# Kernel tuning notes

Hardware: AMD Instinct MI355X
Metric: run time of the kernel (lower is better)

The kernel has to match this reference:

```python
import jax, jax.numpy as jnp
import numpy as np

N_NODES = 1024
N_EDGES = 32768
FEAT = 384
HID = 64
OUT = 64


def setup_inputs() -> dict:
    key = jax.random.key(0)
    ks = jax.random.split(key, 10)
    features = jax.random.normal(ks[0], (N_NODES, FEAT), dtype=jnp.float32)
    edge_index = jax.random.randint(ks[1], (2, N_EDGES), 0, N_NODES, dtype=jnp.int64 if jax.config.jax_enable_x64 else jnp.int32)
    edge_attr = jax.random.uniform(ks[2], (N_EDGES, 1), dtype=jnp.float32)
    # Linear weights (stored as [in, out]; torch Linear does x @ W.T)
    sc = 1.0 / np.sqrt(FEAT)
    Wk = jax.random.uniform(ks[3], (FEAT, HID), dtype=jnp.float32, minval=-sc, maxval=sc)
    Wq = jax.random.uniform(ks[4], (FEAT, HID), dtype=jnp.float32, minval=-sc, maxval=sc)
    Wv = jax.random.uniform(ks[5], (FEAT, OUT), dtype=jnp.float32, minval=-sc, maxval=sc)
    # Embedding tables, init N(0, 1)
    Ek = jax.random.normal(ks[6], (2, HID), dtype=jnp.float32)
    Eq = jax.random.normal(ks[7], (2, HID), dtype=jnp.float32)
    Ev = jax.random.normal(ks[8], (2, OUT), dtype=jnp.float32)
    bias = jnp.full((1,), 0.5, dtype=jnp.float32)
    mult = jnp.full((1,), 10.0, dtype=jnp.float32)
    return {"features": features, "edge_index": edge_index, "edge_attr": edge_attr,
            "Wk": Wk, "Wq": Wq, "Wv": Wv, "Ek": Ek, "Eq": Eq, "Ev": Ev,
            "bias": bias, "mult": mult}


def _dense_adj(src, dst, vals, n, d):
    # torch_geometric.utils.to_dense_adj: scatter-add edge attrs into [N, N, d]
    return jnp.zeros((n, n, d), vals.dtype).at[src, dst].add(vals)


def reference(features, edge_index, edge_attr, Wk, Wq, Wv, Ek, Eq, Ev, bias, mult):
    N, L = features.shape
    k = features @ Wk                      # [N, H]
    q = features @ Wq                      # [N, H]
    v = features @ Wv                      # [N, O]

    # ContinuousEmbeddingIndex: sigmoid interp, weights [E, 2]
    w = jax.nn.sigmoid((edge_attr - bias) * mult)
    w = jnp.concatenate([w, 1.0 - w], axis=-1)

    src, dst = edge_index[0], edge_index[1]
    A = q @ k.T                            # [N, N]

    # key relative embeddings (original casts to int64 -> truncate toward 0)
    rk = jnp.trunc(w @ Ek)                 # [E, H]
    Rk = _dense_adj(src, dst, rk, N, Ek.shape[1])
    A = A + jnp.einsum('ih,ijh->ij', q, Rk)

    # query relative embeddings (also truncated)
    rq = jnp.trunc(w @ Eq)
    Rq = _dense_adj(src, dst, rq, N, Eq.shape[1])
    A = A + jnp.einsum('jh,ijh->ij', k, Rq)

    # term3: (q_repeat * k_repeat).sum(-1) == q @ k.T again
    A = A + q @ k.T

    A = jax.nn.softmax(A / jnp.sqrt(jnp.asarray(L, A.dtype)), axis=-1)
    # dropout is identity at inference
    M = A @ v

    # value relative embeddings (float, no truncation)
    rv = w @ Ev                            # [E, O]
    Rv = _dense_adj(src, dst, rv, N, Ev.shape[1])
    M = M + jnp.einsum('ij,ijd->id', A, Rv)
    return M
```

## Files before the change

kernel.cpp:

```cpp
#include <hip/hip_runtime.h>
#include <math.h>

#define N_NODES 1024
#define N_EDGES 32768
#define FEAT    384
#define INV_S   0.05103103630798287f
#define MAXH    1024

__global__ __launch_bounds__(384) void k_kqv(
        const float* __restrict__ feat,
        const float* __restrict__ Wk, const float* __restrict__ Wq,
        const float* __restrict__ Wv,
        float* __restrict__ q, float* __restrict__ k, float* __restrict__ v) {
    __shared__ float fs[4 * FEAT];
    const int tid = threadIdx.x;
    const int row0 = blockIdx.x * 4;
    ((float4*)fs)[tid] = ((const float4*)(feat + (size_t)row0 * FEAT))[tid];
    __syncthreads();
    const int mat = tid >> 7;
    const int sub = tid & 127;
    const int col = sub & 63;
    const int rh  = sub >> 6;
    const float* W  = (mat == 0) ? Wq : (mat == 1 ? Wk : Wv);
    const float* f0 = fs + (rh * 2) * FEAT;
    const float* f1 = fs + (rh * 2 + 1) * FEAT;
    float a0 = 0.f, a1 = 0.f;
    #pragma unroll 8
    for (int f = 0; f < FEAT; ++f) {
        float wv = W[f * 64 + col];
        a0 = fmaf(f0[f], wv, a0);
        a1 = fmaf(f1[f], wv, a1);
    }
    float* out = (mat == 0) ? q : (mat == 1 ? k : v);
    out[(row0 + rh * 2 + 0) * 64 + col] = a0;
    out[(row0 + rh * 2 + 1) * 64 + col] = a1;
}

__global__ __launch_bounds__(512) void k_mega(
        const float* __restrict__ q, const float* __restrict__ k,
        const float* __restrict__ v,
        const int* __restrict__ ei, const float* __restrict__ eattr,
        const float* __restrict__ Ek, const float* __restrict__ Eq,
        const float* __restrict__ Ev,
        const float* __restrict__ bias, const float* __restrict__ mult,
        float* __restrict__ M) {
    __shared__ __align__(16) float As[4][N_NODES];
    __shared__ float qr[4][64];
    __shared__ __align__(16) float scratch[2048];
    __shared__ float redm[8], reds[8];
    __shared__ float sS[4][2];
    __shared__ int nhit;
    int*   list  = (int*)scratch;
    float* wlist = scratch + 1024;
    float* red   = scratch;

    const int tid  = threadIdx.x;
    const int lane = tid & 63;
    const int wave = tid >> 6;
    const int row0 = blockIdx.x * 4;

    if (tid < 8) ((float*)sS)[tid] = 0.f;
    if (tid == 8) nhit = 0;
    if (tid < 256) qr[tid >> 6][tid & 63] = q[row0 * 64 + tid];
    __syncthreads();

    {
        const int4* s4 = (const int4*)ei;
        #pragma unroll 4
        for (int it = 0; it < 16; ++it) {
            const int i4 = tid + it * 512;
            const int4 sv = s4[i4];
            const int eb = i4 * 4;
            if ((unsigned)(sv.x - row0) < 4u) { int p = atomicAdd(&nhit, 1); if (p < MAXH) list[p] = eb + 0; }
            if ((unsigned)(sv.y - row0) < 4u) { int p = atomicAdd(&nhit, 1); if (p < MAXH) list[p] = eb + 1; }
            if ((unsigned)(sv.z - row0) < 4u) { int p = atomicAdd(&nhit, 1); if (p < MAXH) list[p] = eb + 2; }
            if ((unsigned)(sv.w - row0) < 4u) { int p = atomicAdd(&nhit, 1); if (p < MAXH) list[p] = eb + 3; }
        }
    }

    {
        float qa[4][4];
        #pragma unroll
        for (int r = 0; r < 4; ++r)
            #pragma unroll
            for (int c = 0; c < 4; ++c) qa[r][c] = 0.f;
        #pragma unroll
        for (int jj = 0; jj < 2; ++jj) {
            const int j = tid + jj * 512;
            const float4* kj = (const float4*)(k + (size_t)j * 64);
            float a0 = 0.f, a1 = 0.f, a2 = 0.f, a3 = 0.f;
            #pragma unroll
            for (int kk4 = 0; kk4 < 16; ++kk4) {
                const float4 kv = kj[kk4];
                const float4 q0 = *(const float4*)&qr[0][kk4 * 4];
                const float4 q1 = *(const float4*)&qr[1][kk4 * 4];
                const float4 q2 = *(const float4*)&qr[2][kk4 * 4];
                const float4 q3 = *(const float4*)&qr[3][kk4 * 4];
                a0 = fmaf(q0.x, kv.x, a0); a0 = fmaf(q0.y, kv.y, a0);
                a0 = fmaf(q0.z, kv.z, a0); a0 = fmaf(q0.w, kv.w, a0);
                a1 = fmaf(q1.x, kv.x, a1); a1 = fmaf(q1.y, kv.y, a1);
                a1 = fmaf(q1.z, kv.z, a1); a1 = fmaf(q1.w, kv.w, a1);
                a2 = fmaf(q2.x, kv.x, a2); a2 = fmaf(q2.y, kv.y, a2);
                a2 = fmaf(q2.z, kv.z, a2); a2 = fmaf(q2.w, kv.w, a2);
                a3 = fmaf(q3.x, kv.x, a3); a3 = fmaf(q3.y, kv.y, a3);
                a3 = fmaf(q3.z, kv.z, a3); a3 = fmaf(q3.w, kv.w, a3);
            }
            As[0][j] = 2.f * a0;
            As[1][j] = 2.f * a1;
            As[2][j] = 2.f * a2;
            As[3][j] = 2.f * a3;
        }
        (void)qa;
    }
    __syncthreads();
    const int nh = min(nhit, MAXH);

    {
        const float b0 = bias[0], mu = mult[0];
        const float ek0 = Ek[lane], ek1 = Ek[64 + lane];
        const float eq0 = Eq[lane], eq1 = Eq[64 + lane];
        for (int i = wave; i < nh; i += 8) {
            const int e   = list[i];
            const int src = ei[e], dst = ei[N_EDGES + e];
            const float w  = 1.0f / (1.0f + expf(-(eattr[e] - b0) * mu));
            const float rk = truncf(w * ek0 + (1.0f - w) * ek1);
            const float rq = truncf(w * eq0 + (1.0f - w) * eq1);
            float c = qr[src - row0][lane] * rk + k[(size_t)dst * 64 + lane] * rq;
            #pragma unroll
            for (int off = 32; off >= 1; off >>= 1) c += __shfl_xor(c, off, 64);
            if (lane == 0) {
                atomicAdd(&As[src - row0][dst], c);
                wlist[i] = w;
            }
        }
    }
    __syncthreads();

    const int g  = tid >> 7;
    const int lt = tid & 127;
    {
        float4 x0 = *(float4*)&As[g][lt * 8];
        float4 x1 = *(float4*)&As[g][lt * 8 + 4];
        float m = fmaxf(fmaxf(fmaxf(x0.x, x0.y), fmaxf(x0.z, x0.w)),
                        fmaxf(fmaxf(x1.x, x1.y), fmaxf(x1.z, x1.w)));
        #pragma unroll
        for (int off = 32; off >= 1; off >>= 1) m = fmaxf(m, __shfl_xor(m, off, 64));
        if (lane == 0) redm[wave] = m;
        __syncthreads();
        m = fmaxf(redm[g * 2], redm[g * 2 + 1]);
        float e0 = expf((x0.x - m) * INV_S), e1 = expf((x0.y - m) * INV_S);
        float e2 = expf((x0.z - m) * INV_S), e3 = expf((x0.w - m) * INV_S);
        float e4 = expf((x1.x - m) * INV_S), e5 = expf((x1.y - m) * INV_S);
        float e6 = expf((x1.z - m) * INV_S), e7 = expf((x1.w - m) * INV_S);
        float s = ((e0 + e1) + (e2 + e3)) + ((e4 + e5) + (e6 + e7));
        #pragma unroll
        for (int off = 32; off >= 1; off >>= 1) s += __shfl_xor(s, off, 64);
        if (lane == 0) reds[wave] = s;
        __syncthreads();
        s = reds[g * 2] + reds[g * 2 + 1];
        const float rs = 1.0f / s;
        *(float4*)&As[g][lt * 8]     = make_float4(e0 * rs, e1 * rs, e2 * rs, e3 * rs);
        *(float4*)&As[g][lt * 8 + 4] = make_float4(e4 * rs, e5 * rs, e6 * rs, e7 * rs);
    }
    __syncthreads();

    for (int i = tid; i < nh; i += 512) {
        const int e  = list[i];
        const int rl = ei[e] - row0, dst = ei[N_EDGES + e];
        const float pr = As[rl][dst];
        const float w  = wlist[i];
        atomicAdd(&sS[rl][0], pr * w);
        atomicAdd(&sS[rl][1], pr * (1.0f - w));
    }
    __syncthreads();

    {
        const float* vp = v + (size_t)(wave * 128) * 64 + lane;
        const float* p0 = &As[0][wave * 128];
        const float* p1 = &As[1][wave * 128];
        const float* p2 = &As[2][wave * 128];
        const float* p3 = &As[3][wave * 128];
        float a0 = 0.f, a1 = 0.f, a2 = 0.f, a3 = 0.f;
        #pragma unroll 2
        for (int j4 = 0; j4 < 128; j4 += 4) {
            float4 c0 = *(const float4*)&p0[j4];
            float4 c1 = *(const float4*)&p1[j4];
            float4 c2 = *(const float4*)&p2[j4];
            float4 c3 = *(const float4*)&p3[j4];
            float v0 = vp[(j4 + 0) * 64];
            float v1 = vp[(j4 + 1) * 64];
            float v2 = vp[(j4 + 2) * 64];
            float v3 = vp[(j4 + 3) * 64];
            a0 = fmaf(c0.x, v0, a0); a0 = fmaf(c0.y, v1, a0);
            a0 = fmaf(c0.z, v2, a0); a0 = fmaf(c0.w, v3, a0);
            a1 = fmaf(c1.x, v0, a1); a1 = fmaf(c1.y, v1, a1);
            a1 = fmaf(c1.z, v2, a1); a1 = fmaf(c1.w, v3, a1);
            a2 = fmaf(c2.x, v0, a2); a2 = fmaf(c2.y, v1, a2);
            a2 = fmaf(c2.z, v2, a2); a2 = fmaf(c2.w, v3, a2);
            a3 = fmaf(c3.x, v0, a3); a3 = fmaf(c3.y, v1, a3);
            a3 = fmaf(c3.z, v2, a3); a3 = fmaf(c3.w, v3, a3);
        }
        red[(0 * 8 + wave) * 64 + lane] = a0;
        red[(1 * 8 + wave) * 64 + lane] = a1;
        red[(2 * 8 + wave) * 64 + lane] = a2;
        red[(3 * 8 + wave) * 64 + lane] = a3;
    }
    __syncthreads();
    if (tid < 256) {
        const int r = tid >> 6, d = tid & 63;
        float acc = 0.f;
        #pragma unroll
        for (int w8 = 0; w8 < 8; ++w8) acc += red[(r * 8 + w8) * 64 + d];
        acc += sS[r][0] * Ev[d] + sS[r][1] * Ev[64 + d];
        M[(row0 + r) * 64 + d] = acc;
    }
}

extern "C" void kernel_launch(void* const* d_in, const int* in_sizes, int n_in,
                              void* d_out, int out_size, void* d_ws, size_t ws_size,
                              hipStream_t stream) {
    (void)in_sizes; (void)n_in; (void)out_size; (void)ws_size;
    const float* feat  = (const float*)d_in[0];
    const int*   ei    = (const int*)d_in[1];
    const float* eattr = (const float*)d_in[2];
    const float* Wk    = (const float*)d_in[3];
    const float* Wq    = (const float*)d_in[4];
    const float* Wv    = (const float*)d_in[5];
    const float* Ek    = (const float*)d_in[6];
    const float* Eq    = (const float*)d_in[7];
    const float* Ev    = (const float*)d_in[8];
    const float* bias  = (const float*)d_in[9];
    const float* mult  = (const float*)d_in[10];
    float* M = (float*)d_out;

    float* wsf = (float*)d_ws;
    float* q = wsf;
    float* k = wsf + 65536;
    float* v = wsf + 131072;

    k_kqv<<<256, 384, 0, stream>>>(feat, Wk, Wq, Wv, q, k, v);
    k_mega<<<256, 512, 0, stream>>>(q, k, v, ei, eattr, Ek, Eq, Ev,
                                    bias, mult, M);
}
```

Before: 129.0 us.

## Pre-bucket edges by source block and use transposed K for scores

A new kernel buckets edges by their 4-row source block with global atomics and precomputes the sigmoid weight. This replaces each of 256 blocks scanning all 32768 edges to find its own. The QK stage now reads a transposed copy of k written by the projection kernel, so loads are coalesced, and the main kernel moves to 1024 threads. The change adds one kernel launch and extra workspace, and caps each bucket at 512 entries, which is enough for the average of 128 edges per block.

```diff
diff --git a/kernel.cpp b/kernel.cpp
--- a/kernel.cpp
+++ b/kernel.cpp
@@ -5,16 +5,18 @@
 #define N_EDGES 32768
 #define FEAT    384
 #define INV_S   0.05103103630798287f
-#define MAXH    1024
+#define BCAP    512
 
 __global__ __launch_bounds__(384) void k_kqv(
         const float* __restrict__ feat,
         const float* __restrict__ Wk, const float* __restrict__ Wq,
         const float* __restrict__ Wv,
-        float* __restrict__ q, float* __restrict__ k, float* __restrict__ v) {
+        float* __restrict__ q, float* __restrict__ k, float* __restrict__ v,
+        float* __restrict__ kT, int* __restrict__ cnt) {
     __shared__ float fs[4 * FEAT];
     const int tid = threadIdx.x;
     const int row0 = blockIdx.x * 4;
+    if (blockIdx.x == 0 && tid < 256) cnt[tid] = 0;
     ((float4*)fs)[tid] = ((const float4*)(feat + (size_t)row0 * FEAT))[tid];
     __syncthreads();
     const int mat = tid >> 7;
@@ -34,163 +36,137 @@
     float* out = (mat == 0) ? q : (mat == 1 ? k : v);
     out[(row0 + rh * 2 + 0) * 64 + col] = a0;
     out[(row0 + rh * 2 + 1) * 64 + col] = a1;
-}
-
-__global__ __launch_bounds__(512) void k_mega(
+    if (mat == 1) {
+        kT[col * N_NODES + row0 + rh * 2 + 0] = a0;
+        kT[col * N_NODES + row0 + rh * 2 + 1] = a1;
+    }
+}
+
+__global__ __launch_bounds__(256) void k_bucket(
+        const int* __restrict__ ei, const float* __restrict__ eattr,
+        const float* __restrict__ bias, const float* __restrict__ mult,
+        int* __restrict__ cnt, int* __restrict__ bucket,
+        float* __restrict__ wbuf) {
+    const int e = blockIdx.x * 256 + threadIdx.x;
+    const int src = ei[e], dst = ei[N_EDGES + e];
+    const float w = 1.0f / (1.0f + expf(-(eattr[e] - bias[0]) * mult[0]));
+    const int b = src >> 2;
+    const int pos = atomicAdd(&cnt[b], 1);
+    if (pos < BCAP) {
+        bucket[(b << 9) + pos] = ((src & 3) << 10) | dst;
+        wbuf[(b << 9) + pos] = w;
+    }
+}
+
+__global__ __launch_bounds__(1024) void k_mega(
         const float* __restrict__ q, const float* __restrict__ k,
-        const float* __restrict__ v,
-        const int* __restrict__ ei, const float* __restrict__ eattr,
+        const float* __restrict__ kT, const float* __restrict__ v,
+        const int* __restrict__ cnt, const int* __restrict__ bucket,
+        const float* __restrict__ wbuf,
         const float* __restrict__ Ek, const float* __restrict__ Eq,
-        const float* __restrict__ Ev,
-        const float* __restrict__ bias, const float* __restrict__ mult,
-        float* __restrict__ M) {
+        const float* __restrict__ Ev, float* __restrict__ M) {
     __shared__ __align__(16) float As[4][N_NODES];
     __shared__ float qr[4][64];
-    __shared__ __align__(16) float scratch[2048];
-    __shared__ float redm[8], reds[8];
+    __shared__ float red[4][16][64];
+    __shared__ float redm[16], reds[16];
     __shared__ float sS[4][2];
-    __shared__ int nhit;
-    int*   list  = (int*)scratch;
-    float* wlist = scratch + 1024;
-    float* red   = scratch;
-
+    __shared__ int snh;
     const int tid  = threadIdx.x;
     const int lane = tid & 63;
     const int wave = tid >> 6;
-    const int row0 = blockIdx.x * 4;
+    const int bid  = blockIdx.x;
+    const int row0 = bid * 4;
 
     if (tid < 8) ((float*)sS)[tid] = 0.f;
-    if (tid == 8) nhit = 0;
+    if (tid == 8) snh = min(cnt[bid], BCAP);
     if (tid < 256) qr[tid >> 6][tid & 63] = q[row0 * 64 + tid];
     __syncthreads();
-
-    {
-        const int4* s4 = (const int4*)ei;
-        #pragma unroll 4
-        for (int it = 0; it < 16; ++it) {
-            const int i4 = tid + it * 512;
-            const int4 sv = s4[i4];
-            const int eb = i4 * 4;
-            if ((unsigned)(sv.x - row0) < 4u) { int p = atomicAdd(&nhit, 1); if (p < MAXH) list[p] = eb + 0; }
-            if ((unsigned)(sv.y - row0) < 4u) { int p = atomicAdd(&nhit, 1); if (p < MAXH) list[p] = eb + 1; }
-            if ((unsigned)(sv.z - row0) < 4u) { int p = atomicAdd(&nhit, 1); if (p < MAXH) list[p] = eb + 2; }
-            if ((unsigned)(sv.w - row0) < 4u) { int p = atomicAdd(&nhit, 1); if (p < MAXH) list[p] = eb + 3; }
-        }
-    }
-
-    {
-        float qa[4][4];
-        #pragma unroll
-        for (int r = 0; r < 4; ++r)
-            #pragma unroll
-            for (int c = 0; c < 4; ++c) qa[r][c] = 0.f;
-        #pragma unroll
-        for (int jj = 0; jj < 2; ++jj) {
-            const int j = tid + jj * 512;
-            const float4* kj = (const float4*)(k + (size_t)j * 64);
-            float a0 = 0.f, a1 = 0.f, a2 = 0.f, a3 = 0.f;
-            #pragma unroll
-            for (int kk4 = 0; kk4 < 16; ++kk4) {
-                const float4 kv = kj[kk4];
-                const float4 q0 = *(const float4*)&qr[0][kk4 * 4];
-                const float4 q1 = *(const float4*)&qr[1][kk4 * 4];
-                const float4 q2 = *(const float4*)&qr[2][kk4 * 4];
-                const float4 q3 = *(const float4*)&qr[3][kk4 * 4];
-                a0 = fmaf(q0.x, kv.x, a0); a0 = fmaf(q0.y, kv.y, a0);
-                a0 = fmaf(q0.z, kv.z, a0); a0 = fmaf(q0.w, kv.w, a0);
-                a1 = fmaf(q1.x, kv.x, a1); a1 = fmaf(q1.y, kv.y, a1);
-                a1 = fmaf(q1.z, kv.z, a1); a1 = fmaf(q1.w, kv.w, a1);
-                a2 = fmaf(q2.x, kv.x, a2); a2 = fmaf(q2.y, kv.y, a2);
-                a2 = fmaf(q2.z, kv.z, a2); a2 = fmaf(q2.w, kv.w, a2);
-                a3 = fmaf(q3.x, kv.x, a3); a3 = fmaf(q3.y, kv.y, a3);
-                a3 = fmaf(q3.z, kv.z, a3); a3 = fmaf(q3.w, kv.w, a3);
-            }
-            As[0][j] = 2.f * a0;
-            As[1][j] = 2.f * a1;
-            As[2][j] = 2.f * a2;
-            As[3][j] = 2.f * a3;
-        }
-        (void)qa;
-    }
-    __syncthreads();
-    const int nh = min(nhit, MAXH);
-
-    {
-        const float b0 = bias[0], mu = mult[0];
+    const int nh = snh;
+
+    {
+        const int j = tid;
+        float a0 = 0.f, a1 = 0.f, a2 = 0.f, a3 = 0.f;
+        #pragma unroll
+        for (int kk4 = 0; kk4 < 16; ++kk4) {
+            const float4 q0 = *(const float4*)&qr[0][kk4 * 4];
+            const float4 q1 = *(const float4*)&qr[1][kk4 * 4];
+            const float4 q2 = *(const float4*)&qr[2][kk4 * 4];
+            const float4 q3 = *(const float4*)&qr[3][kk4 * 4];
+            const float kv0 = kT[(kk4 * 4 + 0) * N_NODES + j];
+            const float kv1 = kT[(kk4 * 4 + 1) * N_NODES + j];
+            const float kv2 = kT[(kk4 * 4 + 2) * N_NODES + j];
+            const float kv3 = kT[(kk4 * 4 + 3) * N_NODES + j];
+            a0 = fmaf(q0.x, kv0, a0); a0 = fmaf(q0.y, kv1, a0);
+            a0 = fmaf(q0.z, kv2, a0); a0 = fmaf(q0.w, kv3, a0);
+            a1 = fmaf(q1.x, kv0, a1); a1 = fmaf(q1.y, kv1, a1);
+            a1 = fmaf(q1.z, kv2, a1); a1 = fmaf(q1.w, kv3, a1);
+            a2 = fmaf(q2.x, kv0, a2); a2 = fmaf(q2.y, kv1, a2);
+            a2 = fmaf(q2.z, kv2, a2); a2 = fmaf(q2.w, kv3, a2);
+            a3 = fmaf(q3.x, kv0, a3); a3 = fmaf(q3.y, kv1, a3);
+            a3 = fmaf(q3.z, kv2, a3); a3 = fmaf(q3.w, kv3, a3);
+        }
+        As[0][j] = 2.f * a0;
+        As[1][j] = 2.f * a1;
+        As[2][j] = 2.f * a2;
+        As[3][j] = 2.f * a3;
+    }
+    __syncthreads();
+
+    {
         const float ek0 = Ek[lane], ek1 = Ek[64 + lane];
         const float eq0 = Eq[lane], eq1 = Eq[64 + lane];
-        for (int i = wave; i < nh; i += 8) {
-            const int e   = list[i];
-            const int src = ei[e], dst = ei[N_EDGES + e];
-            const float w  = 1.0f / (1.0f + expf(-(eattr[e] - b0) * mu));
+        for (int i = wave; i < nh; i += 16) {
+            const int ent  = bucket[(bid << 9) + i];
+            const float w  = wbuf[(bid << 9) + i];
+            const int rl = ent >> 10, dst = ent & 1023;
             const float rk = truncf(w * ek0 + (1.0f - w) * ek1);
             const float rq = truncf(w * eq0 + (1.0f - w) * eq1);
-            float c = qr[src - row0][lane] * rk + k[(size_t)dst * 64 + lane] * rq;
+            float c = qr[rl][lane] * rk + k[(size_t)dst * 64 + lane] * rq;
             #pragma unroll
             for (int off = 32; off >= 1; off >>= 1) c += __shfl_xor(c, off, 64);
-            if (lane == 0) {
-                atomicAdd(&As[src - row0][dst], c);
-                wlist[i] = w;
-            }
-        }
-    }
-    __syncthreads();
-
-    const int g  = tid >> 7;
-    const int lt = tid & 127;
-    {
-        float4 x0 = *(float4*)&As[g][lt * 8];
-        float4 x1 = *(float4*)&As[g][lt * 8 + 4];
-        float m = fmaxf(fmaxf(fmaxf(x0.x, x0.y), fmaxf(x0.z, x0.w)),
-                        fmaxf(fmaxf(x1.x, x1.y), fmaxf(x1.z, x1.w)));
+            if (lane == 0) atomicAdd(&As[rl][dst], c);
+        }
+    }
+    __syncthreads();
+
+    {
+        const int g  = tid >> 8;
+        const int lt = tid & 255;
+        float4 x = *(float4*)&As[g][lt * 4];
+        float m = fmaxf(fmaxf(x.x, x.y), fmaxf(x.z, x.w));
         #pragma unroll
         for (int off = 32; off >= 1; off >>= 1) m = fmaxf(m, __shfl_xor(m, off, 64));
         if (lane == 0) redm[wave] = m;
         __syncthreads();
-        m = fmaxf(redm[g * 2], redm[g * 2 + 1]);
-        float e0 = expf((x0.x - m) * INV_S), e1 = expf((x0.y - m) * INV_S);
-        float e2 = expf((x0.z - m) * INV_S), e3 = expf((x0.w - m) * INV_S);
-        float e4 = expf((x1.x - m) * INV_S), e5 = expf((x1.y - m) * INV_S);
-        float e6 = expf((x1.z - m) * INV_S), e7 = expf((x1.w - m) * INV_S);
-        float s = ((e0 + e1) + (e2 + e3)) + ((e4 + e5) + (e6 + e7));
+        m = fmaxf(fmaxf(redm[g * 4 + 0], redm[g * 4 + 1]),
+                  fmaxf(redm[g * 4 + 2], redm[g * 4 + 3]));
+        float e0 = expf((x.x - m) * INV_S), e1 = expf((x.y - m) * INV_S);
+        float e2 = expf((x.z - m) * INV_S), e3 = expf((x.w - m) * INV_S);
+        float s = (e0 + e1) + (e2 + e3);
         #pragma unroll
         for (int off = 32; off >= 1; off >>= 1) s += __shfl_xor(s, off, 64);
         if (lane == 0) reds[wave] = s;
         __syncthreads();
-        s = reds[g * 2] + reds[g * 2 + 1];
+        s = (reds[g * 4 + 0] + reds[g * 4 + 1]) + (reds[g * 4 + 2] + reds[g * 4 + 3]);
         const float rs = 1.0f / s;
-        *(float4*)&As[g][lt * 8]     = make_float4(e0 * rs, e1 * rs, e2 * rs, e3 * rs);
-        *(float4*)&As[g][lt * 8 + 4] = make_float4(e4 * rs, e5 * rs, e6 * rs, e7 * rs);
-    }
-    __syncthreads();
-
-    for (int i = tid; i < nh; i += 512) {
-        const int e  = list[i];
-        const int rl = ei[e] - row0, dst = ei[N_EDGES + e];
-        const float pr = As[rl][dst];
-        const float w  = wlist[i];
-        atomicAdd(&sS[rl][0], pr * w);
-        atomicAdd(&sS[rl][1], pr * (1.0f - w));
-    }
-    __syncthreads();
-
-    {
-        const float* vp = v + (size_t)(wave * 128) * 64 + lane;
-        const float* p0 = &As[0][wave * 128];
-        const float* p1 = &As[1][wave * 128];
-        const float* p2 = &As[2][wave * 128];
-        const float* p3 = &As[3][wave * 128];
+        *(float4*)&As[g][lt * 4] = make_float4(e0 * rs, e1 * rs, e2 * rs, e3 * rs);
+    }
+    __syncthreads();
+
+    {
+        const int jb = wave * 64;
+        const float* vp = v + (size_t)jb * 64 + lane;
         float a0 = 0.f, a1 = 0.f, a2 = 0.f, a3 = 0.f;
-        #pragma unroll 2
-        for (int j4 = 0; j4 < 128; j4 += 4) {
-            float4 c0 = *(const float4*)&p0[j4];
-            float4 c1 = *(const float4*)&p1[j4];
-            float4 c2 = *(const float4*)&p2[j4];
-            float4 c3 = *(const float4*)&p3[j4];
-            float v0 = vp[(j4 + 0) * 64];
-            float v1 = vp[(j4 + 1) * 64];
-            float v2 = vp[(j4 + 2) * 64];
-            float v3 = vp[(j4 + 3) * 64];
+        #pragma unroll 4
+        for (int j4 = 0; j4 < 64; j4 += 4) {
+            const float4 c0 = *(const float4*)&As[0][jb + j4];
+            const float4 c1 = *(const float4*)&As[1][jb + j4];
+            const float4 c2 = *(const float4*)&As[2][jb + j4];
+            const float4 c3 = *(const float4*)&As[3][jb + j4];
+            const float v0 = vp[(j4 + 0) * 64];
+            const float v1 = vp[(j4 + 1) * 64];
+            const float v2 = vp[(j4 + 2) * 64];
+            const float v3 = vp[(j4 + 3) * 64];
             a0 = fmaf(c0.x, v0, a0); a0 = fmaf(c0.y, v1, a0);
             a0 = fmaf(c0.z, v2, a0); a0 = fmaf(c0.w, v3, a0);
             a1 = fmaf(c1.x, v0, a1); a1 = fmaf(c1.y, v1, a1);
@@ -200,17 +176,27 @@
             a3 = fmaf(c3.x, v0, a3); a3 = fmaf(c3.y, v1, a3);
             a3 = fmaf(c3.z, v2, a3); a3 = fmaf(c3.w, v3, a3);
         }
-        red[(0 * 8 + wave) * 64 + lane] = a0;
-        red[(1 * 8 + wave) * 64 + lane] = a1;
-        red[(2 * 8 + wave) * 64 + lane] = a2;
-        red[(3 * 8 + wave) * 64 + lane] = a3;
-    }
-    __syncthreads();
+        red[0][wave][lane] = a0;
+        red[1][wave][lane] = a1;
+        red[2][wave][lane] = a2;
+        red[3][wave][lane] = a3;
+
+        for (int i = tid; i < nh; i += 1024) {
+            const int ent  = bucket[(bid << 9) + i];
+            const float w  = wbuf[(bid << 9) + i];
+            const int rl = ent >> 10, dst = ent & 1023;
+            const float pr = As[rl][dst];
+            atomicAdd(&sS[rl][0], pr * w);
+            atomicAdd(&sS[rl][1], pr * (1.0f - w));
+        }
+    }
+    __syncthreads();
+
     if (tid < 256) {
         const int r = tid >> 6, d = tid & 63;
         float acc = 0.f;
         #pragma unroll
-        for (int w8 = 0; w8 < 8; ++w8) acc += red[(r * 8 + w8) * 64 + d];
+        for (int w16 = 0; w16 < 16; ++w16) acc += red[r][w16][d];
         acc += sS[r][0] * Ev[d] + sS[r][1] * Ev[64 + d];
         M[(row0 + r) * 64 + d] = acc;
     }
@@ -234,11 +220,17 @@
     float* M = (float*)d_out;
 
     float* wsf = (float*)d_ws;
-    float* q = wsf;
-    float* k = wsf + 65536;
-    float* v = wsf + 131072;
-
-    k_kqv<<<256, 384, 0, stream>>>(feat, Wk, Wq, Wv, q, k, v);
-    k_mega<<<256, 512, 0, stream>>>(q, k, v, ei, eattr, Ek, Eq, Ev,
-                                    bias, mult, M);
-}
+    float* q    = wsf;
+    float* k    = wsf + 65536;
+    float* v    = wsf + 131072;
+    float* kT   = wsf + 196608;
+    float* wbuf = wsf + 262144;
+    int* ibase  = (int*)(wsf + 393216);
+    int* cnt    = ibase;
+    int* bucket = ibase + 256;
+
+    k_kqv<<<256, 384, 0, stream>>>(feat, Wk, Wq, Wv, q, k, v, kT, cnt);
+    k_bucket<<<128, 256, 0, stream>>>(ei, eattr, bias, mult, cnt, bucket, wbuf);
+    k_mega<<<256, 1024, 0, stream>>>(q, k, kT, v, cnt, bucket, wbuf,
+                                     Ek, Eq, Ev, M);
+}
```

Measured after the change: 123.6 us. -4.2%, faster.
